# Kernel tuning notes

Measured on AMD Instinct MI355X. Metric: run time of the kernel, lower is better.

The kernel has to match this reference:

```python
import jax, jax.numpy as jnp
import numpy as np

N_NODES = 50000
N_EDGES = 800000
IN_CH = 128
HID = 64
HEADS = 2
OUT_CH = 3
N_GRAPHS = 64
NEG_SLOPE = 0.2


def _gatv2(x, src, dst, Wl, Wr, att, bias, heads, out_ch, concat, n_nodes):
    # GATv2Conv (PyG semantics, eval mode, self-loops already appended)
    xl = (x @ Wl).reshape(n_nodes, heads, out_ch)  # lin_l -> source messages
    xr = (x @ Wr).reshape(n_nodes, heads, out_ch)  # lin_r -> target side
    e = jax.nn.leaky_relu(xl[src] + xr[dst], NEG_SLOPE)          # [E, H, C]
    alpha = jnp.einsum('ehc,hc->eh', e, att)                     # [E, H]
    # segment softmax over incoming edges of each target node
    amax = jax.ops.segment_max(alpha, dst, num_segments=n_nodes)  # [N, H]
    ea = jnp.exp(alpha - amax[dst])
    denom = jax.ops.segment_sum(ea, dst, num_segments=n_nodes)
    alpha = ea / (denom[dst] + 1e-16)
    msg = xl[src] * alpha[..., None]                             # [E, H, C]
    out = jax.ops.segment_sum(msg, dst, num_segments=n_nodes)    # [N, H, C]
    out = out.reshape(n_nodes, heads * out_ch) if concat else out.mean(axis=1)
    return out + bias


def setup_inputs() -> dict:
    key = jax.random.key(0)
    ks = jax.random.split(key, 12)
    x = jax.random.normal(ks[0], (N_NODES, IN_CH), dtype=jnp.float32)
    edge_index = jax.random.randint(ks[1], (2, N_EDGES), 0, N_NODES, dtype=jnp.int64 if jax.config.jax_enable_x64 else jnp.int32)
    batch = jnp.sort(jax.random.randint(ks[2], (N_NODES,), 0, N_GRAPHS))
    s = 0.05
    params = {
        'W1l': jax.random.normal(ks[3], (IN_CH, HEADS * HID), dtype=jnp.float32) * s,
        'W1r': jax.random.normal(ks[4], (IN_CH, HEADS * HID), dtype=jnp.float32) * s,
        'att1': jax.random.normal(ks[5], (HEADS, HID), dtype=jnp.float32) * s,
        'b1': jnp.zeros((HEADS * HID,), dtype=jnp.float32),
        'W2l': jax.random.normal(ks[6], (HEADS * HID, OUT_CH), dtype=jnp.float32) * s,
        'W2r': jax.random.normal(ks[7], (HEADS * HID, OUT_CH), dtype=jnp.float32) * s,
        'att2': jax.random.normal(ks[8], (1, OUT_CH), dtype=jnp.float32) * s,
        'b2': jnp.zeros((OUT_CH,), dtype=jnp.float32),
        'Wr1': jax.random.normal(ks[9], (OUT_CH, 64), dtype=jnp.float32) * s,
        'br1': jnp.zeros((64,), dtype=jnp.float32),
        'Wr2': jax.random.normal(ks[10], (64, 3), dtype=jnp.float32) * s,
        'br2': jnp.zeros((3,), dtype=jnp.float32),
    }
    return {'x': x, 'edge_index': edge_index, 'batch': batch, **params}


def reference(x, edge_index, batch, W1l, W1r, att1, b1, W2l, W2r, att2, b2, Wr1, br1, Wr2, br2):
    n = x.shape[0]
    loops = jnp.arange(n, dtype=edge_index.dtype)
    src = jnp.concatenate([edge_index[0], loops])  # add_self_loops=True
    dst = jnp.concatenate([edge_index[1], loops])
    h = _gatv2(x, src, dst, W1l, W1r, att1, b1, HEADS, HID, True, n)
    h = jax.nn.elu(h)
    h = _gatv2(h, src, dst, W2l, W2r, att2, b2, 1, OUT_CH, False, n)
    # global_mean_pool over graphs
    sums = jax.ops.segment_sum(h, batch, num_segments=N_GRAPHS)
    cnt = jax.ops.segment_sum(jnp.ones((n,), h.dtype), batch, num_segments=N_GRAPHS)
    g = sums / jnp.maximum(cnt, 1.0)[:, None]
    g = jax.nn.relu(g @ Wr1 + br1)
    return g @ Wr2 + br2
```

## Files before the change

### kernel.cpp

```cpp
#include <hip/hip_runtime.h>


#define NGRAPH 64
#define LOG2E 1.4426950408889634f

typedef __attribute__((ext_vector_type(2))) _Float16 hf2;

#define DPP_ROR(C, x) \
  __int_as_float(__builtin_amdgcn_update_dpp(0, __float_as_int(x), (0x120 | C), 0xF, 0xF, false))
#define DPP_QUAD(C, x) \
  __int_as_float(__builtin_amdgcn_update_dpp(0, __float_as_int(x), (C), 0xF, 0xF, false))

__device__ __forceinline__ float rowsum16(float v) {
  v += DPP_ROR(8, v);
  v += DPP_ROR(4, v);
  v += DPP_ROR(2, v);
  v += DPP_ROR(1, v);
  return v;
}

__device__ __forceinline__ unsigned bf16rne(float f) {
  unsigned u = __float_as_uint(f);
  return (u + 0x7FFFu + ((u >> 16) & 1u)) >> 16;
}

__device__ __forceinline__ unsigned short f16u(float f) {
  union { _Float16 h; unsigned short u; } v;
  v.h = (_Float16)f;
  return v.u;
}

__device__ __forceinline__ hf2 as_hf2(unsigned u) {
  union { unsigned u; hf2 h; } v;
  v.u = u;
  return v.h;
}

typedef __attribute__((ext_vector_type(8))) short bf16x8;
typedef __attribute__((ext_vector_type(4))) float f32x4;

__global__ void k_deg(const int* __restrict__ ei, int E, int Et,
                      int* __restrict__ deg, int* __restrict__ rank) {
  int e = blockIdx.x * blockDim.x + threadIdx.x;
  if (e >= Et) return;
  int d = (e < E) ? ei[E + e] : (e - E);
  rank[e] = atomicAdd(&deg[d], 1);
}

__global__ __launch_bounds__(256) void k_scan_part(const int* __restrict__ deg,
                                                   int* __restrict__ bsum, int n) {
  __shared__ int sd[256];
  int t = threadIdx.x;
  int i = blockIdx.x * 1024 + t * 4;
  int s = 0;
  if (i + 4 <= n) {
    int4 d = *(const int4*)&deg[i];
    s = d.x + d.y + d.z + d.w;
  } else {
    for (int j = i; j < min(i + 4, n); ++j) s += deg[j];
  }
  sd[t] = s;
  __syncthreads();
  for (int off = 128; off; off >>= 1) {
    if (t < off) sd[t] += sd[t + off];
    __syncthreads();
  }
  if (t == 0) bsum[blockIdx.x] = sd[0];
}

__global__ __launch_bounds__(64) void k_scan_top(int* __restrict__ bsum, int nb) {
  __shared__ int s[64];
  int t = threadIdx.x;
  s[t] = (t < nb) ? bsum[t] : 0;
  __syncthreads();
  int acc = 0;
  for (int j = 0; j < t; ++j) acc += s[j];
  if (t < nb) bsum[t] = acc;
}

__global__ __launch_bounds__(256) void k_scan_write(const int* __restrict__ deg,
                                                    const int* __restrict__ bsum,
                                                    int* __restrict__ row_ptr, int n) {
  __shared__ int sd[256];
  int t = threadIdx.x;
  int i = blockIdx.x * 1024 + t * 4;
  int4 d = make_int4(0, 0, 0, 0);
  bool full = (i + 4 <= n);
  if (full) d = *(const int4*)&deg[i];
  else {
    if (i + 0 < n) d.x = deg[i + 0];
    if (i + 1 < n) d.y = deg[i + 1];
    if (i + 2 < n) d.z = deg[i + 2];
    if (i + 3 < n) d.w = deg[i + 3];
  }
  int s = d.x + d.y + d.z + d.w;
  sd[t] = s;
  __syncthreads();
  for (int off = 1; off < 256; off <<= 1) {
    int v = (t >= off) ? sd[t - off] : 0;
    __syncthreads();
    sd[t] += v;
    __syncthreads();
  }
  int ex = sd[t] - s + bsum[blockIdx.x];
  int4 r;
  r.x = ex;
  r.y = ex + d.x;
  r.z = r.y + d.y;
  r.w = r.z + d.z;
  if (full) {
    *(int4*)&row_ptr[i] = r;
    if (i + 4 == n) row_ptr[n] = r.w + d.w;
  } else if (i < n) {
    int run = ex;
    int vals[4] = {d.x, d.y, d.z, d.w};
    for (int j = 0; j < 4 && i + j < n; ++j) {
      row_ptr[i + j] = run;
      run += vals[j];
    }
    if (i <= n && i + 4 > n) row_ptr[n] = run;
  }
}

__global__ void k_fill(const int* __restrict__ ei, int E, int Et,
                       const int* __restrict__ row_ptr,
                       const int* __restrict__ rank,
                       int* __restrict__ csr_src) {
  int e = blockIdx.x * blockDim.x + threadIdx.x;
  if (e >= Et) return;
  int s, d;
  if (e < E) { s = ei[e]; d = ei[E + e]; }
  else       { s = e - E; d = s; }
  csr_src[row_ptr[d] + rank[e]] = s;
}

__global__ __launch_bounds__(256) void k_cvtw(const float* __restrict__ W1l,
                                              const float* __restrict__ W1r,
                                              unsigned short* __restrict__ whp,
                                              unsigned short* __restrict__ wlp) {
  int t = threadIdx.x;
  int kc = t >> 6;
  int l = t & 63;
  int lr = l & 15;
  int k0 = kc * 32 + ((l >> 4) << 3);
  int b = blockIdx.x;
  int col = b * 16 + lr;
  float f[8];
#pragma unroll
  for (int j = 0; j < 8; ++j)
    f[j] = (col < 128) ? W1l[(size_t)(k0 + j) * 128 + col]
                       : W1r[(size_t)(k0 + j) * 128 + (col - 128)];
  unsigned hv[8], lv[8];
#pragma unroll
  for (int j = 0; j < 8; ++j) {
    hv[j] = bf16rne(f[j]);
    float r = f[j] - __uint_as_float(hv[j] << 16);
    lv[j] = bf16rne(r);
  }
  uint4 ph, pl;
  ph.x = hv[0] | (hv[1] << 16); ph.y = hv[2] | (hv[3] << 16);
  ph.z = hv[4] | (hv[5] << 16); ph.w = hv[6] | (hv[7] << 16);
  pl.x = lv[0] | (lv[1] << 16); pl.y = lv[2] | (lv[3] << 16);
  pl.z = lv[4] | (lv[5] << 16); pl.w = lv[6] | (lv[7] << 16);
  size_t slot = (((size_t)b * 4 + kc) * 64 + l) * 8;
  *(uint4*)&whp[slot] = ph;
  *(uint4*)&wlp[slot] = pl;
}

__global__ __launch_bounds__(256) void k_gmfma(const float* __restrict__ x,
                                               const unsigned short* __restrict__ whp,
                                               const unsigned short* __restrict__ wlp,
                                               unsigned short* __restrict__ outl,
                                               unsigned short* __restrict__ outr, int n) {
  __shared__ __align__(16) unsigned short xh_lds[2 * 4 * 64 * 8];
  __shared__ __align__(16) unsigned short xl_lds[2 * 4 * 64 * 8];
  int t = threadIdx.x;
  int skc = t >> 6;
  int sl = t & 63;
  int slr = sl & 15;
  int sk0 = skc * 32 + ((sl >> 4) << 3);
  int r0 = blockIdx.x * 32;

#pragma unroll
  for (int rb = 0; rb < 2; ++rb) {
    int row = r0 + rb * 16 + slr;
    float f[8];
    if (row < n) {
      float4 a = *(const float4*)&x[(size_t)row * 128 + sk0];
      float4 c = *(const float4*)&x[(size_t)row * 128 + sk0 + 4];
      f[0] = a.x; f[1] = a.y; f[2] = a.z; f[3] = a.w;
      f[4] = c.x; f[5] = c.y; f[6] = c.z; f[7] = c.w;
    } else {
#pragma unroll
      for (int j = 0; j < 8; ++j) f[j] = 0.f;
    }
    unsigned hv[8], lv[8];
#pragma unroll
    for (int j = 0; j < 8; ++j) {
      hv[j] = bf16rne(f[j]);
      float r = f[j] - __uint_as_float(hv[j] << 16);
      lv[j] = bf16rne(r);
    }
    uint4 ph, pl;
    ph.x = hv[0] | (hv[1] << 16); ph.y = hv[2] | (hv[3] << 16);
    ph.z = hv[4] | (hv[5] << 16); ph.w = hv[6] | (hv[7] << 16);
    pl.x = lv[0] | (lv[1] << 16); pl.y = lv[2] | (lv[3] << 16);
    pl.z = lv[4] | (lv[5] << 16); pl.w = lv[6] | (lv[7] << 16);
    int slot = ((rb * 4 + skc) * 64 + sl) * 8;
    *(uint4*)&xh_lds[slot] = ph;
    *(uint4*)&xl_lds[slot] = pl;
  }
  __syncthreads();

  int w = t >> 6;
  int lane = t & 63;
  int lr = lane & 15;

  f32x4 acc[2][4] = {};

#pragma unroll
  for (int kc = 0; kc < 4; ++kc) {
    bf16x8 ah[2], al[2], bh[4], bl[4];
#pragma unroll
    for (int m = 0; m < 2; ++m) {
      int slot = ((m * 4 + kc) * 64 + lane) * 8;
      ah[m] = *(const bf16x8*)&xh_lds[slot];
      al[m] = *(const bf16x8*)&xl_lds[slot];
    }
#pragma unroll
    for (int f = 0; f < 4; ++f) {
      size_t slot = (((size_t)(w * 4 + f) * 4 + kc) * 64 + lane) * 8;
      bh[f] = *(const bf16x8*)&whp[slot];
      bl[f] = *(const bf16x8*)&wlp[slot];
    }
#pragma unroll
    for (int m = 0; m < 2; ++m)
#pragma unroll
      for (int f = 0; f < 4; ++f) {
        acc[m][f] = __builtin_amdgcn_mfma_f32_16x16x32_bf16(ah[m], bh[f], acc[m][f], 0, 0, 0);
        acc[m][f] = __builtin_amdgcn_mfma_f32_16x16x32_bf16(ah[m], bl[f], acc[m][f], 0, 0, 0);
        acc[m][f] = __builtin_amdgcn_mfma_f32_16x16x32_bf16(al[m], bh[f], acc[m][f], 0, 0, 0);
      }
  }

  int rbase = (lane >> 4) * 4;
  unsigned short* dst = (w < 2) ? outl : outr;
  int cb = (w & 1) * 64;
#pragma unroll
  for (int m = 0; m < 2; ++m)
#pragma unroll
    for (int f = 0; f < 4; ++f) {
      int col = cb + f * 16 + lr;
#pragma unroll
      for (int i = 0; i < 4; ++i) {
        int row = r0 + m * 16 + rbase + i;
        if (row < n)
          dst[(size_t)row * 128 + col] = f16u(acc[m][f][i]);
      }
    }
}

__global__ __launch_bounds__(256) void k_fused1(const unsigned short* __restrict__ xl,
                                                const unsigned short* __restrict__ xr,
                                                const int* __restrict__ row_ptr,
                                                const int* __restrict__ csr_src,
                                                const float* __restrict__ att1,
                                                const float* __restrict__ b1,
                                                const float* __restrict__ W2l,
                                                const float* __restrict__ W2r,
                                                float* __restrict__ xl2,
                                                float* __restrict__ xr2, int n) {
  int wid  = (blockIdx.x * 256 + threadIdx.x) >> 6;
  int lane = threadIdx.x & 63;
  int sub  = lane & 31;
  int node = min(wid * 2 + (lane >> 5), n - 1);
  int ch = sub * 4;
  const char* xlb = (const char*)xl;
  unsigned chb = (unsigned)sub * 8u;

  uint2 xrq = *(const uint2*)&xr[(size_t)node * 128 + ch];
  hf2 xr01 = as_hf2(xrq.x), xr23 = as_hf2(xrq.y);
  float4 atv = *(const float4*)&att1[ch];
  hf2 at01, at23;
  at01.x = (_Float16)(atv.x * LOG2E); at01.y = (_Float16)(atv.y * LOG2E);
  at23.x = (_Float16)(atv.z * LOG2E); at23.y = (_Float16)(atv.w * LOG2E);
  hf2 k02; k02.x = (_Float16)0.2f; k02.y = (_Float16)0.2f;

  int s0 = row_ptr[node];
  int deg = row_ptr[node + 1] - s0;
  int odeg = __shfl_xor(deg, 32);
  int mindeg = min(deg, odeg);
  int maxdeg = max(deg, odeg);
  const int* sp = csr_src + s0;

  float m = -1e30f, l = 0.f;
  float4 acc = make_float4(0.f, 0.f, 0.f, 0.f);

#define EDGE(p, x0, x1, x2, x3, q)                                      \
    { hf2 v01 = as_hf2(q.x), v23 = as_hf2(q.y);                         \
      hf2 t01 = v01 + xr01, t23 = v23 + xr23;                           \
      hf2 l01 = __builtin_elementwise_max(t01, t01 * k02);              \
      hf2 l23 = __builtin_elementwise_max(t23, t23 * k02);              \
      p = __builtin_amdgcn_fdot2(l23, at23,                             \
            __builtin_amdgcn_fdot2(l01, at01, 0.f, false), false);      \
      x0 = (float)v01.x; x1 = (float)v01.y;                             \
      x2 = (float)v23.x; x3 = (float)v23.y; }

#define BODY(CLAMPED)                                                   \
  {                                                                     \
    int sA, sB, sC, sD;                                                 \
    if (CLAMPED) {                                                      \
      int dm1 = deg - 1;                                                \
      sA = sp[min(e + 0, dm1)];                                         \
      sB = sp[min(e + 1, dm1)];                                         \
      sC = sp[min(e + 2, dm1)];                                         \
      sD = sp[min(e + 3, dm1)];                                         \
    } else {                                                            \
      sA = sp[e + 0]; sB = sp[e + 1]; sC = sp[e + 2]; sD = sp[e + 3];   \
    }                                                                   \
    uint2 qa = *(const uint2*)(xlb + (((unsigned)sA << 8) + chb));      \
    uint2 qb = *(const uint2*)(xlb + (((unsigned)sB << 8) + chb));      \
    uint2 qc = *(const uint2*)(xlb + (((unsigned)sC << 8) + chb));      \
    uint2 qd = *(const uint2*)(xlb + (((unsigned)sD << 8) + chb));      \
    float pa, pb, pc, pd;                                               \
    float xa0, xa1, xa2, xa3, xb0, xb1, xb2, xb3;                       \
    float xc0, xc1, xc2, xc3, xd0, xd1, xd2, xd3;                       \
    EDGE(pa, xa0, xa1, xa2, xa3, qa)                                    \
    EDGE(pb, xb0, xb1, xb2, xb3, qb)                                    \
    EDGE(pc, xc0, xc1, xc2, xc3, qc)                                    \
    EDGE(pd, xd0, xd1, xd2, xd3, qd)                                    \
    pa = rowsum16(pa);                                                  \
    pb = rowsum16(pb);                                                  \
    pc = rowsum16(pc);                                                  \
    pd = rowsum16(pd);                                                  \
    if (CLAMPED) {                                                      \
      pa = (e + 0 < deg) ? pa : -1e30f;                                 \
      pb = (e + 1 < deg) ? pb : -1e30f;                                 \
      pc = (e + 2 < deg) ? pc : -1e30f;                                 \
      pd = (e + 3 < deg) ? pd : -1e30f;                                 \
    }                                                                   \
    float mn = fmaxf(m, fmaxf(fmaxf(pa, pb), fmaxf(pc, pd)));           \
    float sc = exp2f(m - mn);                                           \
    float wa = exp2f(pa - mn);                                          \
    float wb = exp2f(pb - mn);                                          \
    float wc = exp2f(pc - mn);                                          \
    float wd = exp2f(pd - mn);                                          \
    acc.x = fmaf(wd, xd0, fmaf(wc, xc0, fmaf(wb, xb0, fmaf(wa, xa0, acc.x * sc)))); \
    acc.y = fmaf(wd, xd1, fmaf(wc, xc1, fmaf(wb, xb1, fmaf(wa, xa1, acc.y * sc)))); \
    acc.z = fmaf(wd, xd2, fmaf(wc, xc2, fmaf(wb, xb2, fmaf(wa, xa2, acc.z * sc)))); \
    acc.w = fmaf(wd, xd3, fmaf(wc, xc3, fmaf(wb, xb3, fmaf(wa, xa3, acc.w * sc)))); \
    l = fmaf(l, sc, wa + wb + wc + wd);                                 \
    m = mn;                                                             \
  }

  int e = 0;
  for (; e + 4 <= mindeg; e += 4) BODY(false)
  for (; e < maxdeg; e += 4) BODY(true)
#undef BODY
#undef EDGE

  float inv = 1.f / (l + 1e-16f);
  float4 b1v = *(const float4*)&b1[ch];
  float4 h;
  h.x = acc.x * inv + b1v.x; h.x = h.x > 0.f ? h.x : expm1f(h.x);
  h.y = acc.y * inv + b1v.y; h.y = h.y > 0.f ? h.y : expm1f(h.y);
  h.z = acc.z * inv + b1v.z; h.z = h.z > 0.f ? h.z : expm1f(h.z);
  h.w = acc.w * inv + b1v.w; h.w = h.w > 0.f ? h.w : expm1f(h.w);

  float4 u0 = *(const float4*)&W2l[ch * 3 + 0];
  float4 u1 = *(const float4*)&W2l[ch * 3 + 4];
  float4 u2 = *(const float4*)&W2l[ch * 3 + 8];
  float al0 = fmaf(h.w, u2.y, fmaf(h.z, u1.z, fmaf(h.y, u0.w, h.x * u0.x)));
  float al1 = fmaf(h.w, u2.z, fmaf(h.z, u1.w, fmaf(h.y, u1.x, h.x * u0.y)));
  float al2 = fmaf(h.w, u2.w, fmaf(h.z, u2.x, fmaf(h.y, u1.y, h.x * u0.z)));
  float4 v0 = *(const float4*)&W2r[ch * 3 + 0];
  float4 v1 = *(const float4*)&W2r[ch * 3 + 4];
  float4 v2 = *(const float4*)&W2r[ch * 3 + 8];
  float ar0 = fmaf(h.w, v2.y, fmaf(h.z, v1.z, fmaf(h.y, v0.w, h.x * v0.x)));
  float ar1 = fmaf(h.w, v2.z, fmaf(h.z, v1.w, fmaf(h.y, v1.x, h.x * v0.y)));
  float ar2 = fmaf(h.w, v2.w, fmaf(h.z, v2.x, fmaf(h.y, v1.y, h.x * v0.z)));
#pragma unroll
  for (int off = 1; off < 32; off <<= 1) {
    al0 += __shfl_xor(al0, off); al1 += __shfl_xor(al1, off);
    al2 += __shfl_xor(al2, off); ar0 += __shfl_xor(ar0, off);
    ar1 += __shfl_xor(ar1, off); ar2 += __shfl_xor(ar2, off);
  }
  if (sub == 0 && wid * 2 + (lane >> 5) < n) {
    *(float4*)&xl2[node * 4] = make_float4(al0, al1, al2, 0.f);
    *(float4*)&xr2[node * 4] = make_float4(ar0, ar1, ar2, 0.f);
  }
}

__global__ __launch_bounds__(256) void k_fused2(const float* __restrict__ xl2,
                                                const float* __restrict__ xr2,
                                                const int* __restrict__ row_ptr,
                                                const int* __restrict__ csr_src,
                                                const float* __restrict__ att2,
                                                const float* __restrict__ b2,
                                                const int* __restrict__ batch,
                                                float* __restrict__ gsum,
                                                float* __restrict__ gcnt, int n) {
  __shared__ float ls[NGRAPH * 3];
  __shared__ float lc[NGRAPH];
  int t = threadIdx.x;
  for (int i = t; i < NGRAPH * 3; i += 256) ls[i] = 0.f;
  for (int i = t; i < NGRAPH; i += 256) lc[i] = 0.f;
  __syncthreads();

  int node = (blockIdx.x * 256 + t) >> 2;
  int lane = t & 3;
  if (node < n) {
    float4 xrv = *(const float4*)&xr2[node * 4];
    float c0 = att2[0] * LOG2E, c1 = att2[1] * LOG2E, c2 = att2[2] * LOG2E;
    int s0 = row_ptr[node], s1 = row_ptr[node + 1];
    float m = -1e30f, l = 0.f, a0 = 0.f, a1 = 0.f, a2 = 0.f;
    for (int slot = s0 + lane; slot < s1; slot += 4) {
      int s = csr_src[slot];
      float4 xlv = *(const float4*)&xl2[s * 4];
      float t0 = xlv.x + xrv.x; t0 = fmaxf(t0, 0.2f * t0);
      float t1 = xlv.y + xrv.y; t1 = fmaxf(t1, 0.2f * t1);
      float t2 = xlv.z + xrv.z; t2 = fmaxf(t2, 0.2f * t2);
      float p = fmaf(t2, c2, fmaf(t1, c1, t0 * c0));
      float mn = fmaxf(m, p);
      float sc = exp2f(m - mn);
      float w  = exp2f(p - mn);
      a0 = a0 * sc + w * xlv.x;
      a1 = a1 * sc + w * xlv.y;
      a2 = a2 * sc + w * xlv.z;
      l = l * sc + w;
      m = mn;
    }
#define MERGEQ(C)                                                       \
    {                                                                   \
      float m2 = DPP_QUAD(C, m);                                        \
      float l2 = DPP_QUAD(C, l);                                        \
      float b0 = DPP_QUAD(C, a0);                                       \
      float b1v = DPP_QUAD(C, a1);                                      \
      float b2v = DPP_QUAD(C, a2);                                      \
      float mn = fmaxf(m, m2);                                          \
      float sA = exp2f(m - mn);                                         \
      float sB = exp2f(m2 - mn);                                        \
      a0 = a0 * sA + b0 * sB;                                           \
      a1 = a1 * sA + b1v * sB;                                          \
      a2 = a2 * sA + b2v * sB;                                          \
      l = l * sA + l2 * sB;                                             \
      m = mn;                                                           \
    }
    MERGEQ(0x39) MERGEQ(0x4E)
#undef MERGEQ
    if (lane == 0) {
      float inv = 1.f / (l + 1e-16f);
      float o0 = a0 * inv + b2[0];
      float o1 = a1 * inv + b2[1];
      float o2 = a2 * inv + b2[2];
      int b = batch[node];
      atomicAdd(&ls[b * 3 + 0], o0);
      atomicAdd(&ls[b * 3 + 1], o1);
      atomicAdd(&ls[b * 3 + 2], o2);
      atomicAdd(&lc[b], 1.f);
    }
  }
  __syncthreads();
  for (int i = t; i < NGRAPH * 3; i += 256)
    if (ls[i] != 0.f) atomicAdd(&gsum[i], ls[i]);
  for (int i = t; i < NGRAPH; i += 256)
    if (lc[i] != 0.f) atomicAdd(&gcnt[i], lc[i]);
}

__global__ __launch_bounds__(64) void k_mlp(const float* __restrict__ gsum,
                                            const float* __restrict__ gcnt,
                                            const float* __restrict__ Wr1,
                                            const float* __restrict__ br1,
                                            const float* __restrict__ Wr2,
                                            const float* __restrict__ br2,
                                            float* __restrict__ out) {
  int t = threadIdx.x;
  if (t >= NGRAPH) return;
  float cnt = fmaxf(gcnt[t], 1.f);
  float g0 = gsum[t * 3 + 0] / cnt;
  float g1 = gsum[t * 3 + 1] / cnt;
  float g2 = gsum[t * 3 + 2] / cnt;
  float o0 = br2[0], o1 = br2[1], o2 = br2[2];
  for (int j = 0; j < 64; ++j) {
    float hj = g0 * Wr1[j] + g1 * Wr1[64 + j] + g2 * Wr1[128 + j] + br1[j];
    hj = fmaxf(hj, 0.f);
    o0 = fmaf(hj, Wr2[j * 3 + 0], o0);
    o1 = fmaf(hj, Wr2[j * 3 + 1], o1);
    o2 = fmaf(hj, Wr2[j * 3 + 2], o2);
  }
  out[t * 3 + 0] = o0;
  out[t * 3 + 1] = o1;
  out[t * 3 + 2] = o2;
}

extern "C" void kernel_launch(void* const* d_in, const int* in_sizes, int n_in,
                              void* d_out, int out_size, void* d_ws, size_t ws_size,
                              hipStream_t stream) {
  const float* x    = (const float*)d_in[0];
  const int*   ei   = (const int*)d_in[1];
  const int*   batch= (const int*)d_in[2];
  const float* W1l  = (const float*)d_in[3];
  const float* W1r  = (const float*)d_in[4];
  const float* att1 = (const float*)d_in[5];
  const float* b1   = (const float*)d_in[6];
  const float* W2l  = (const float*)d_in[7];
  const float* W2r  = (const float*)d_in[8];
  const float* att2 = (const float*)d_in[9];
  const float* b2   = (const float*)d_in[10];
  const float* Wr1  = (const float*)d_in[11];
  const float* br1  = (const float*)d_in[12];
  const float* Wr2  = (const float*)d_in[13];
  const float* br2  = (const float*)d_in[14];
  float* out = (float*)d_out;

  const int N  = in_sizes[0] / 128;
  const int E  = in_sizes[1] / 2;
  const int Et = E + N;
  const int NB = (N + 1023) / 1024;
  const int NB32 = (N + 31) / 32;

  char* p = (char*)d_ws;
  auto alloc = [&](size_t bytes) -> char* {
    char* r = p;
    p += (bytes + 255) & ~(size_t)255;
    return r;
  };
  unsigned short* xl1 = (unsigned short*)alloc((size_t)N * 128 * 2);
  unsigned short* xr1 = (unsigned short*)alloc((size_t)N * 128 * 2);
  int*      row_ptr= (int*)alloc((size_t)(N + 1) * 4);
  int*      csr_src= (int*)alloc((size_t)Et * 4);
  int*      rank   = (int*)alloc((size_t)Et * 4);
  int*      bsum   = (int*)alloc(64 * 4);
  char*     z0     = p;
  int*      deg    = (int*)alloc((size_t)N * 4);
  float*    gsum   = (float*)alloc(NGRAPH * 3 * 4);
  float*    gcnt   = (float*)alloc(NGRAPH * 4);
  size_t    zbytes = (size_t)(p - z0);
  float*    xl2    = (float*)alloc((size_t)N * 4 * 4);
  float*    xr2    = (float*)alloc((size_t)N * 4 * 4);
  unsigned short* whp = (unsigned short*)alloc((size_t)16 * 2048 * 2);
  unsigned short* wlp = (unsigned short*)alloc((size_t)16 * 2048 * 2);

  hipMemsetAsync(z0, 0, zbytes, stream);
  hipLaunchKernelGGL(k_deg, dim3((Et + 255) / 256), dim3(256), 0, stream,
                     ei, E, Et, deg, rank);
  hipLaunchKernelGGL(k_scan_part, dim3(NB), dim3(256), 0, stream, deg, bsum, N);
  hipLaunchKernelGGL(k_scan_top, dim3(1), dim3(64), 0, stream, bsum, NB);
  hipLaunchKernelGGL(k_scan_write, dim3(NB), dim3(256), 0, stream,
                     deg, bsum, row_ptr, N);
  hipLaunchKernelGGL(k_fill, dim3((Et + 255) / 256), dim3(256), 0, stream,
                     ei, E, Et, row_ptr, rank, csr_src);
  hipLaunchKernelGGL(k_cvtw, dim3(16), dim3(256), 0, stream,
                     W1l, W1r, whp, wlp);
  hipLaunchKernelGGL(k_gmfma, dim3(NB32), dim3(256), 0, stream,
                     x, whp, wlp, xl1, xr1, N);
  int waves1 = (N + 1) / 2;
  hipLaunchKernelGGL(k_fused1, dim3((waves1 * 64 + 255) / 256), dim3(256), 0, stream,
                     xl1, xr1, row_ptr, csr_src, att1, b1, W2l, W2r, xl2, xr2, N);
  hipLaunchKernelGGL(k_fused2, dim3((N * 4 + 255) / 256), dim3(256), 0, stream,
                     xl2, xr2, row_ptr, csr_src, att2, b2, batch, gsum, gcnt, N);
  hipLaunchKernelGGL(k_mlp, dim3(1), dim3(64), 0, stream,
                     gsum, gcnt, Wr1, br1, Wr2, br2, out);
}
```

Before: 238.9 us.

## Fold scan-top into scan-write and software-pipeline edge gathers in layer-1 kernel

The separate single-block k_scan_top kernel is removed. Each k_scan_write block now computes its own prefix offset with a wave-level shuffle reduction over the partial block sums, saving one kernel launch. Separately, the fused layer-1 GAT kernel's edge loop is restructured to prefetch the next four neighbour feature rows while the current four are processed. It replaces the split unclamped/clamped loops with one clamped loop. This aims to hide gather latency, at the cost of clamping every iteration, a wasted prefetch at the end, and more live registers.

```diff
diff --git a/kernel.cpp b/kernel.cpp
--- a/kernel.cpp
+++ b/kernel.cpp
@@ -68,21 +68,19 @@
   if (t == 0) bsum[blockIdx.x] = sd[0];
 }
 
-__global__ __launch_bounds__(64) void k_scan_top(int* __restrict__ bsum, int nb) {
-  __shared__ int s[64];
-  int t = threadIdx.x;
-  s[t] = (t < nb) ? bsum[t] : 0;
-  __syncthreads();
-  int acc = 0;
-  for (int j = 0; j < t; ++j) acc += s[j];
-  if (t < nb) bsum[t] = acc;
-}
-
 __global__ __launch_bounds__(256) void k_scan_write(const int* __restrict__ deg,
                                                     const int* __restrict__ bsum,
-                                                    int* __restrict__ row_ptr, int n) {
+                                                    int* __restrict__ row_ptr,
+                                                    int n, int nb) {
   __shared__ int sd[256];
+  __shared__ int boff;
   int t = threadIdx.x;
+  if (t < 64) {
+    int v = (t < nb && t < (int)blockIdx.x) ? bsum[t] : 0;
+#pragma unroll
+    for (int off = 32; off; off >>= 1) v += __shfl_xor(v, off);
+    if (t == 0) boff = v;
+  }
   int i = blockIdx.x * 1024 + t * 4;
   int4 d = make_int4(0, 0, 0, 0);
   bool full = (i + 4 <= n);
@@ -102,7 +100,7 @@
     sd[t] += v;
     __syncthreads();
   }
-  int ex = sd[t] - s + bsum[blockIdx.x];
+  int ex = sd[t] - s + boff;
   int4 r;
   r.x = ex;
   r.y = ex + d.x;
@@ -289,8 +287,8 @@
   int s0 = row_ptr[node];
   int deg = row_ptr[node + 1] - s0;
   int odeg = __shfl_xor(deg, 32);
-  int mindeg = min(deg, odeg);
   int maxdeg = max(deg, odeg);
+  int dm1 = deg - 1;
   const int* sp = csr_src + s0;
 
   float m = -1e30f, l = 0.f;
@@ -306,57 +304,59 @@
       x0 = (float)v01.x; x1 = (float)v01.y;                             \
       x2 = (float)v23.x; x3 = (float)v23.y; }
 
-#define BODY(CLAMPED)                                                   \
-  {                                                                     \
-    int sA, sB, sC, sD;                                                 \
-    if (CLAMPED) {                                                      \
-      int dm1 = deg - 1;                                                \
-      sA = sp[min(e + 0, dm1)];                                         \
-      sB = sp[min(e + 1, dm1)];                                         \
-      sC = sp[min(e + 2, dm1)];                                         \
-      sD = sp[min(e + 3, dm1)];                                         \
-    } else {                                                            \
-      sA = sp[e + 0]; sB = sp[e + 1]; sC = sp[e + 2]; sD = sp[e + 3];   \
-    }                                                                   \
-    uint2 qa = *(const uint2*)(xlb + (((unsigned)sA << 8) + chb));      \
-    uint2 qb = *(const uint2*)(xlb + (((unsigned)sB << 8) + chb));      \
-    uint2 qc = *(const uint2*)(xlb + (((unsigned)sC << 8) + chb));      \
-    uint2 qd = *(const uint2*)(xlb + (((unsigned)sD << 8) + chb));      \
-    float pa, pb, pc, pd;                                               \
-    float xa0, xa1, xa2, xa3, xb0, xb1, xb2, xb3;                       \
-    float xc0, xc1, xc2, xc3, xd0, xd1, xd2, xd3;                       \
-    EDGE(pa, xa0, xa1, xa2, xa3, qa)                                    \
-    EDGE(pb, xb0, xb1, xb2, xb3, qb)                                    \
-    EDGE(pc, xc0, xc1, xc2, xc3, qc)                                    \
-    EDGE(pd, xd0, xd1, xd2, xd3, qd)                                    \
-    pa = rowsum16(pa);                                                  \
-    pb = rowsum16(pb);                                                  \
-    pc = rowsum16(pc);                                                  \
-    pd = rowsum16(pd);                                                  \
-    if (CLAMPED) {                                                      \
-      pa = (e + 0 < deg) ? pa : -1e30f;                                 \
-      pb = (e + 1 < deg) ? pb : -1e30f;                                 \
-      pc = (e + 2 < deg) ? pc : -1e30f;                                 \
-      pd = (e + 3 < deg) ? pd : -1e30f;                                 \
-    }                                                                   \
-    float mn = fmaxf(m, fmaxf(fmaxf(pa, pb), fmaxf(pc, pd)));           \
-    float sc = exp2f(m - mn);                                           \
-    float wa = exp2f(pa - mn);                                          \
-    float wb = exp2f(pb - mn);                                          \
-    float wc = exp2f(pc - mn);                                          \
-    float wd = exp2f(pd - mn);                                          \
-    acc.x = fmaf(wd, xd0, fmaf(wc, xc0, fmaf(wb, xb0, fmaf(wa, xa0, acc.x * sc)))); \
-    acc.y = fmaf(wd, xd1, fmaf(wc, xc1, fmaf(wb, xb1, fmaf(wa, xa1, acc.y * sc)))); \
-    acc.z = fmaf(wd, xd2, fmaf(wc, xc2, fmaf(wb, xb2, fmaf(wa, xa2, acc.z * sc)))); \
-    acc.w = fmaf(wd, xd3, fmaf(wc, xc3, fmaf(wb, xb3, fmaf(wa, xa3, acc.w * sc)))); \
-    l = fmaf(l, sc, wa + wb + wc + wd);                                 \
-    m = mn;                                                             \
-  }
-
-  int e = 0;
-  for (; e + 4 <= mindeg; e += 4) BODY(false)
-  for (; e < maxdeg; e += 4) BODY(true)
-#undef BODY
+  uint2 q0, q1, q2, q3;
+  {
+    int sA = sp[0];
+    int sB = sp[min(1, dm1)];
+    int sC = sp[min(2, dm1)];
+    int sD = sp[min(3, dm1)];
+    q0 = *(const uint2*)(xlb + (((unsigned)sA << 8) + chb));
+    q1 = *(const uint2*)(xlb + (((unsigned)sB << 8) + chb));
+    q2 = *(const uint2*)(xlb + (((unsigned)sC << 8) + chb));
+    q3 = *(const uint2*)(xlb + (((unsigned)sD << 8) + chb));
+  }
+
+  for (int e = 0; e < maxdeg; e += 4) {
+    int en = e + 4;
+    int sA = sp[min(en + 0, dm1)];
+    int sB = sp[min(en + 1, dm1)];
+    int sC = sp[min(en + 2, dm1)];
+    int sD = sp[min(en + 3, dm1)];
+    uint2 f0 = *(const uint2*)(xlb + (((unsigned)sA << 8) + chb));
+    uint2 f1 = *(const uint2*)(xlb + (((unsigned)sB << 8) + chb));
+    uint2 f2 = *(const uint2*)(xlb + (((unsigned)sC << 8) + chb));
+    uint2 f3 = *(const uint2*)(xlb + (((unsigned)sD << 8) + chb));
+
+    float pa, pb, pc, pd;
+    float xa0, xa1, xa2, xa3, xb0, xb1, xb2, xb3;
+    float xc0, xc1, xc2, xc3, xd0, xd1, xd2, xd3;
+    EDGE(pa, xa0, xa1, xa2, xa3, q0)
+    EDGE(pb, xb0, xb1, xb2, xb3, q1)
+    EDGE(pc, xc0, xc1, xc2, xc3, q2)
+    EDGE(pd, xd0, xd1, xd2, xd3, q3)
+    pa = rowsum16(pa);
+    pb = rowsum16(pb);
+    pc = rowsum16(pc);
+    pd = rowsum16(pd);
+    pa = (e + 0 < deg) ? pa : -1e30f;
+    pb = (e + 1 < deg) ? pb : -1e30f;
+    pc = (e + 2 < deg) ? pc : -1e30f;
+    pd = (e + 3 < deg) ? pd : -1e30f;
+    float mn = fmaxf(m, fmaxf(fmaxf(pa, pb), fmaxf(pc, pd)));
+    float sc = exp2f(m - mn);
+    float wa = exp2f(pa - mn);
+    float wb = exp2f(pb - mn);
+    float wc = exp2f(pc - mn);
+    float wd = exp2f(pd - mn);
+    acc.x = fmaf(wd, xd0, fmaf(wc, xc0, fmaf(wb, xb0, fmaf(wa, xa0, acc.x * sc))));
+    acc.y = fmaf(wd, xd1, fmaf(wc, xc1, fmaf(wb, xb1, fmaf(wa, xa1, acc.y * sc))));
+    acc.z = fmaf(wd, xd2, fmaf(wc, xc2, fmaf(wb, xb2, fmaf(wa, xa2, acc.z * sc))));
+    acc.w = fmaf(wd, xd3, fmaf(wc, xc3, fmaf(wb, xb3, fmaf(wa, xa3, acc.w * sc))));
+    l = fmaf(l, sc, wa + wb + wc + wd);
+    m = mn;
+
+    q0 = f0; q1 = f1; q2 = f2; q3 = f3;
+  }
 #undef EDGE
 
   float inv = 1.f / (l + 1e-16f);
@@ -545,9 +545,8 @@
   hipLaunchKernelGGL(k_deg, dim3((Et + 255) / 256), dim3(256), 0, stream,
                      ei, E, Et, deg, rank);
   hipLaunchKernelGGL(k_scan_part, dim3(NB), dim3(256), 0, stream, deg, bsum, N);
-  hipLaunchKernelGGL(k_scan_top, dim3(1), dim3(64), 0, stream, bsum, NB);
   hipLaunchKernelGGL(k_scan_write, dim3(NB), dim3(256), 0, stream,
-                     deg, bsum, row_ptr, N);
+                     deg, bsum, row_ptr, N, NB);
   hipLaunchKernelGGL(k_fill, dim3((Et + 255) / 256), dim3(256), 0, stream,
                      ei, E, Et, row_ptr, rank, csr_src);
   hipLaunchKernelGGL(k_cvtw, dim3(16), dim3(256), 0, stream,
```

New measurement: 237.2 us. No clear change (-0.7%).
